# Performance work log

Measured on AMD Instinct MI355X. Metric: run time of the kernel, lower is better.

## Reference

```python
import jax, jax.numpy as jnp
import numpy as np

NUM_HEADS = 8


def setup_inputs() -> dict:
    key0 = jax.random.key(0)
    ks = jax.random.split(key0, 12)
    N, M, B, C = 512, 512, 1, 256
    inp = {
        "query": jax.random.normal(ks[0], (N, B, C), dtype=jnp.float32),
        "key": jax.random.normal(ks[1], (M, B, C), dtype=jnp.float32),
        "value": jax.random.normal(ks[2], (M, B, C), dtype=jnp.float32),
        "embed_g": jax.random.normal(ks[3], (B, N, M, C), dtype=jnp.float32),
        "Wq": jax.random.normal(ks[4], (C, C), dtype=jnp.float32) * 0.02,
        "bq": jnp.zeros((C,), dtype=jnp.float32),
        "Wk": jax.random.normal(ks[5], (C, C), dtype=jnp.float32) * 0.02,
        "bk": jnp.zeros((C,), dtype=jnp.float32),
        "Wv": jax.random.normal(ks[6], (C, C), dtype=jnp.float32) * 0.02,
        "bv": jnp.zeros((C,), dtype=jnp.float32),
        "Wg": jax.random.normal(ks[7], (C, C), dtype=jnp.float32) * 0.02,
        "bg": jnp.zeros((C,), dtype=jnp.float32),
    }
    return inp


def reference(query, key, value, embed_g, Wq, bq, Wk, bk, Wv, bv, Wg, bg):
    H = NUM_HEADS
    N, B, C = query.shape
    M = key.shape[0]
    Dh = C // H

    # torch nn.Linear: x @ W.T + b
    q = (query @ Wq.T + bq).reshape(N, B, H, Dh).transpose(1, 2, 0, 3)   # (B,H,N,Dh)
    k = (key @ Wk.T + bk).reshape(M, B, H, Dh).transpose(1, 2, 0, 3)     # (B,H,M,Dh)
    v = (value @ Wv.T + bv).reshape(M, B, H, Dh).transpose(1, 2, 0, 3)   # (B,H,M,Dh)
    g = (embed_g @ Wg.T + bg).reshape(B, N, M, H, Dh).transpose(0, 3, 1, 2, 4)  # (B,H,N,M,Dh)

    scores_p = jnp.einsum('bhnc,bhnmc->bhnm', q, g)
    scores_e = jnp.einsum('bhnc,bhmc->bhnm', q, k)
    scores = (scores_e + scores_p) / jnp.sqrt(jnp.asarray(Dh, dtype=q.dtype))
    attn = jax.nn.softmax(scores, axis=-1)                               # (B,H,N,M)

    hidden = jnp.einsum('bhnm,bhmd->bhnd', attn, v)                      # (B,H,N,Dh)
    hidden = hidden.transpose(0, 2, 1, 3).reshape(B, N, C)               # (B,N,C)
    hidden = hidden.transpose(1, 0, 2)                                   # (N,B,C)
    return hidden, attn
```

## Files before the change

### kernel.cpp

```cpp
#include <hip/hip_runtime.h>


template <int CTRL, int RMASK>
__device__ __forceinline__ float dpp_add(float v) {
  int x = __builtin_amdgcn_update_dpp(0, __float_as_int(v), CTRL, RMASK, 0xf, false);
  return v + __int_as_float(x);
}

__global__ __launch_bounds__(256) void k_transpose(const float* __restrict__ Wq,
                                                   const float* __restrict__ Wk,
                                                   const float* __restrict__ Wv,
                                                   float* __restrict__ wt) {
  const float* W = (blockIdx.y == 0) ? Wq : (blockIdx.y == 1) ? Wk : Wv;
  float* O = wt + (size_t)blockIdx.y * 65536;
  __shared__ float t[64][65];
  const int tile = blockIdx.x;
  const int tr = (tile >> 2) * 64, tc = (tile & 3) * 64;
  const int c = threadIdx.x & 63, r0 = threadIdx.x >> 6;
#pragma unroll
  for (int i = 0; i < 16; ++i) {
    int r = r0 + i * 4;
    t[r][c] = W[(tr + r) * 256 + tc + c];
  }
  __syncthreads();
#pragma unroll
  for (int i = 0; i < 16; ++i) {
    int r = r0 + i * 4;
    O[(tc + r) * 256 + tr + c] = t[c][r];
  }
}

__global__ __launch_bounds__(256) void k_proj(const float* __restrict__ q_in,
                                              const float* __restrict__ k_in,
                                              const float* __restrict__ v_in,
                                              const float* __restrict__ bq,
                                              const float* __restrict__ bk,
                                              const float* __restrict__ bv,
                                              const float* __restrict__ wt,
                                              float* __restrict__ outb) {
  const int mat = blockIdx.y;
  const float* x = mat == 0 ? q_in : mat == 1 ? k_in : v_in;
  const float* b = mat == 0 ? bq : mat == 1 ? bk : bv;
  const float* WT = wt + (size_t)mat * 65536;
  float* out = outb + (size_t)mat * 131072;

  __shared__ float xl[8][256];
  const int tid = threadIdx.x;
  const int n0 = blockIdx.x * 8;
  for (int idx = tid; idx < 2048; idx += 256)
    xl[idx >> 8][idx & 255] = x[(n0 + (idx >> 8)) * 256 + (idx & 255)];
  __syncthreads();

  float acc[8] = {0.f, 0.f, 0.f, 0.f, 0.f, 0.f, 0.f, 0.f};
  for (int j = 0; j < 256; j += 4) {
    const float w0 = WT[(j + 0) * 256 + tid];
    const float w1 = WT[(j + 1) * 256 + tid];
    const float w2 = WT[(j + 2) * 256 + tid];
    const float w3 = WT[(j + 3) * 256 + tid];
#pragma unroll
    for (int r = 0; r < 8; ++r) {
      const float4 xv = *(const float4*)&xl[r][j];
      acc[r] += xv.x * w0 + xv.y * w1 + xv.z * w2 + xv.w * w3;
    }
  }
  const float bb = b[tid];
#pragma unroll
  for (int r = 0; r < 8; ++r) out[(n0 + r) * 256 + tid] = acc[r] + bb;
}

__global__ __launch_bounds__(256) void k_tfold(const float* __restrict__ qkv,
                                               const float* __restrict__ Wg,
                                               const float* __restrict__ bg,
                                               float* __restrict__ t_ws,
                                               float* __restrict__ qb_ws) {
  const int h = blockIdx.y;
  const int n0 = blockIdx.x * 64;
  const int tid = threadIdx.x;
  __shared__ float wg_s[32][256];
  __shared__ float qs[64][32];
  __shared__ float bgs[32];

  for (int idx = tid; idx < 8192; idx += 256)
    wg_s[idx >> 8][idx & 255] = Wg[(size_t)(h * 32 + (idx >> 8)) * 256 + (idx & 255)];
  for (int idx = tid; idx < 2048; idx += 256)
    qs[idx >> 5][idx & 31] = qkv[(size_t)(n0 + (idx >> 5)) * 256 + h * 32 + (idx & 31)];
  if (tid < 32) bgs[tid] = bg[h * 32 + tid];
  __syncthreads();

  float wr[32];
#pragma unroll
  for (int i = 0; i < 32; ++i) wr[i] = wg_s[i][tid];
  for (int nn = 0; nn < 64; ++nn) {
    float a = 0.f;
#pragma unroll
    for (int i = 0; i < 32; ++i) a = fmaf(qs[nn][i], wr[i], a);
    t_ws[(size_t)(n0 + nn) * 2048 + h * 256 + tid] = a;
  }
  if (tid < 64) {
    float a = 0.f;
#pragma unroll
    for (int i = 0; i < 32; ++i) a = fmaf(qs[tid][i], bgs[i], a);
    qb_ws[(n0 + tid) * 8 + h] = a;
  }
}

__global__ __launch_bounds__(256) void k_scores(const float* __restrict__ Eg,
                                                const float* __restrict__ qkv,
                                                const float* __restrict__ t_ws,
                                                const float* __restrict__ qb_ws,
                                                float* __restrict__ attn_raw) {
  const int n = blockIdx.x, mb = blockIdx.y;
  const int tid = threadIdx.x;
  const int lane = tid & 63, w = tid >> 6;
  const int s = lane & 31, g = lane >> 5;
  const float* k_g = qkv + 131072;

  __shared__ float p_lds[1024];

  float t_r[8][8];
#pragma unroll
  for (int h = 0; h < 8; ++h) {
    const float4 a = *(const float4*)(t_ws + (size_t)n * 2048 + h * 256 + s * 8);
    const float4 b = *(const float4*)(t_ws + (size_t)n * 2048 + h * 256 + s * 8 + 4);
    t_r[h][0] = a.x; t_r[h][1] = a.y; t_r[h][2] = a.z; t_r[h][3] = a.w;
    t_r[h][4] = b.x; t_r[h][5] = b.y; t_r[h][6] = b.z; t_r[h][7] = b.w;
  }
  float q_r[8];
  {
    const float4 a = *(const float4*)(qkv + n * 256 + s * 8);
    const float4 b = *(const float4*)(qkv + n * 256 + s * 8 + 4);
    q_r[0] = a.x; q_r[1] = a.y; q_r[2] = a.z; q_r[3] = a.w;
    q_r[4] = b.x; q_r[5] = b.y; q_r[6] = b.z; q_r[7] = b.w;
  }
  float qb_r[8];
#pragma unroll
  for (int h = 0; h < 8; ++h) qb_r[h] = qb_ws[n * 8 + h];
  float msk[8];
#pragma unroll
  for (int h = 0; h < 8; ++h) msk[h] = ((s >> 2) == h) ? 1.f : 0.f;

  const float scale = 0.17677669529663687f;

  const int row0 = mb * 128 + w * 32 + g;
  const float* E0 = Eg + ((size_t)n * 512 + row0) * 256 + s * 8;
  const float* K0 = k_g + (size_t)row0 * 256 + s * 8;
  int mo = w * 32 + g;

#pragma unroll 2
  for (int it = 0; it < 16; ++it) {
    const float4 e0 = *(const float4*)(E0);
    const float4 e1 = *(const float4*)(E0 + 4);
    const float4 k0 = *(const float4*)(K0);
    const float4 k1 = *(const float4*)(K0 + 4);
    float kacc;
    kacc = k0.x * q_r[0];             kacc = fmaf(k0.y, q_r[1], kacc);
    kacc = fmaf(k0.z, q_r[2], kacc);  kacc = fmaf(k0.w, q_r[3], kacc);
    kacc = fmaf(k1.x, q_r[4], kacc);  kacc = fmaf(k1.y, q_r[5], kacc);
    kacc = fmaf(k1.z, q_r[6], kacc);  kacc = fmaf(k1.w, q_r[7], kacc);
#pragma unroll
    for (int h = 0; h < 8; ++h) {
      float v = msk[h] * kacc;
      v = fmaf(e0.x, t_r[h][0], v); v = fmaf(e0.y, t_r[h][1], v);
      v = fmaf(e0.z, t_r[h][2], v); v = fmaf(e0.w, t_r[h][3], v);
      v = fmaf(e1.x, t_r[h][4], v); v = fmaf(e1.y, t_r[h][5], v);
      v = fmaf(e1.z, t_r[h][6], v); v = fmaf(e1.w, t_r[h][7], v);
      v = dpp_add<0xB1, 0xf>(v);
      v = dpp_add<0x4E, 0xf>(v);
      v = dpp_add<0x141, 0xf>(v);
      v = dpp_add<0x140, 0xf>(v);
      v = dpp_add<0x142, 0xa>(v);
      v = (v + qb_r[h]) * scale;
      if (s == 16 + h) p_lds[h * 128 + mo] = v;
    }
    E0 += 512; K0 += 512; mo += 2;
  }
  __syncthreads();
  for (int idx = tid; idx < 1024; idx += 256)
    attn_raw[(size_t)(idx >> 7) * 262144 + n * 512 + mb * 128 + (idx & 127)] = p_lds[idx];
}

__global__ __launch_bounds__(512) void k_finish(const float* __restrict__ qkv,
                                                float* __restrict__ out) {
  const float* v_g = qkv + 262144;
  const int n = blockIdx.x, tid = threadIdx.x;
  const int lane = tid & 63, w = tid >> 6;
  float* attn = out + 131072;

  __shared__ float sc[4096];
  __shared__ float invd[8];
  __shared__ float pv[2][256];

  {
    float4* d = (float4*)sc;
    int i0 = tid;
    d[i0] = *(const float4*)(attn + (size_t)(i0 >> 7) * 262144 + n * 512 + (i0 & 127) * 4);
    int i1 = tid + 512;
    d[i1] = *(const float4*)(attn + (size_t)(i1 >> 7) * 262144 + n * 512 + (i1 & 127) * 4);
  }
  __syncthreads();

  {
    float vals[8];
#pragma unroll
    for (int i = 0; i < 8; ++i) vals[i] = sc[w * 512 + lane + i * 64];
    float mx = vals[0];
#pragma unroll
    for (int i = 1; i < 8; ++i) mx = fmaxf(mx, vals[i]);
#pragma unroll
    for (int off = 1; off < 64; off <<= 1) mx = fmaxf(mx, __shfl_xor(mx, off));
    float sum = 0.f;
#pragma unroll
    for (int i = 0; i < 8; ++i) {
      const float e = __expf(vals[i] - mx);
      sum += e;
      sc[w * 512 + lane + i * 64] = e;
    }
#pragma unroll
    for (int off = 1; off < 64; off <<= 1) sum += __shfl_xor(sum, off);
    if (lane == 0) invd[w] = 1.f / sum;
  }
  __syncthreads();

#pragma unroll
  for (int r = 0; r < 8; ++r) {
    const int idx = tid + r * 512;
    const int h = idx >> 9, m = idx & 511;
    attn[(size_t)h * 262144 + n * 512 + m] = sc[idx] * invd[h];
  }

  const int c = tid & 255, half = tid >> 8, h2 = c >> 5;
  const float* pr = sc + h2 * 512 + half * 256;
  const float* vp = v_g + (size_t)half * 65536 + c;
  float acc = 0.f;
#pragma unroll 4
  for (int m4 = 0; m4 < 64; ++m4) {
    const float4 p4 = *(const float4*)(pr + m4 * 4);
    const int mb = m4 * 4;
    acc = fmaf(p4.x, vp[(size_t)(mb + 0) * 256], acc);
    acc = fmaf(p4.y, vp[(size_t)(mb + 1) * 256], acc);
    acc = fmaf(p4.z, vp[(size_t)(mb + 2) * 256], acc);
    acc = fmaf(p4.w, vp[(size_t)(mb + 3) * 256], acc);
  }
  pv[half][c] = acc;
  __syncthreads();
  if (tid < 256) out[n * 256 + tid] = (pv[0][tid] + pv[1][tid]) * invd[tid >> 5];
}

extern "C" void kernel_launch(void* const* d_in, const int* in_sizes, int n_in,
                              void* d_out, int out_size, void* d_ws, size_t ws_size,
                              hipStream_t stream) {
  const float* query = (const float*)d_in[0];
  const float* key   = (const float*)d_in[1];
  const float* value = (const float*)d_in[2];
  const float* Eg    = (const float*)d_in[3];
  const float* Wq    = (const float*)d_in[4];
  const float* bq    = (const float*)d_in[5];
  const float* Wk    = (const float*)d_in[6];
  const float* bk    = (const float*)d_in[7];
  const float* Wv    = (const float*)d_in[8];
  const float* bv    = (const float*)d_in[9];
  const float* Wg    = (const float*)d_in[10];
  const float* bg    = (const float*)d_in[11];
  float* out = (float*)d_out;

  float* ws = (float*)d_ws;
  float* wt = ws;
  float* qkv = wt + 3 * 65536;
  float* t_ws = qkv + 3 * 131072;
  float* qb_ws = t_ws + 512 * 2048;

  k_transpose<<<dim3(16, 3), 256, 0, stream>>>(Wq, Wk, Wv, wt);
  k_proj<<<dim3(64, 3), 256, 0, stream>>>(query, key, value, bq, bk, bv, wt, qkv);
  k_tfold<<<dim3(8, 8), 256, 0, stream>>>(qkv, Wg, bg, t_ws, qb_ws);
  k_scores<<<dim3(512, 4), 256, 0, stream>>>(Eg, qkv, t_ws, qb_ws, out + 131072);
  k_finish<<<dim3(512), 512, 0, stream>>>(qkv, out);
}
```

Before: 113.1 us.

## Move q·k score term from scores kernel into finish kernel

Takes the q·k dot product out of the bandwidth-bound scores kernel and computes it once per (n,m) pair in the finish kernel, adding it into the shared-memory scores before the softmax. Previously every query row's block reloaded K and ran the per-head masked multiplies. The softmax scale is folded into t_ws and qb_ws in tfold and into q in finish, and the scores loop is unrolled more. The cost is an extra K read pass and one more barrier in the finish kernel.

```diff
diff --git a/kernel.cpp b/kernel.cpp
--- a/kernel.cpp
+++ b/kernel.cpp
@@ -76,6 +76,7 @@
   const int h = blockIdx.y;
   const int n0 = blockIdx.x * 64;
   const int tid = threadIdx.x;
+  const float scale = 0.17677669529663687f;
   __shared__ float wg_s[32][256];
   __shared__ float qs[64][32];
   __shared__ float bgs[32];
@@ -94,18 +95,17 @@
     float a = 0.f;
 #pragma unroll
     for (int i = 0; i < 32; ++i) a = fmaf(qs[nn][i], wr[i], a);
-    t_ws[(size_t)(n0 + nn) * 2048 + h * 256 + tid] = a;
+    t_ws[(size_t)(n0 + nn) * 2048 + h * 256 + tid] = a * scale;
   }
   if (tid < 64) {
     float a = 0.f;
 #pragma unroll
     for (int i = 0; i < 32; ++i) a = fmaf(qs[tid][i], bgs[i], a);
-    qb_ws[(n0 + tid) * 8 + h] = a;
+    qb_ws[(n0 + tid) * 8 + h] = a * scale;
   }
 }
 
 __global__ __launch_bounds__(256) void k_scores(const float* __restrict__ Eg,
-                                                const float* __restrict__ qkv,
                                                 const float* __restrict__ t_ws,
                                                 const float* __restrict__ qb_ws,
                                                 float* __restrict__ attn_raw) {
@@ -113,7 +113,6 @@
   const int tid = threadIdx.x;
   const int lane = tid & 63, w = tid >> 6;
   const int s = lane & 31, g = lane >> 5;
-  const float* k_g = qkv + 131072;
 
   __shared__ float p_lds[1024];
 
@@ -125,54 +124,34 @@
     t_r[h][0] = a.x; t_r[h][1] = a.y; t_r[h][2] = a.z; t_r[h][3] = a.w;
     t_r[h][4] = b.x; t_r[h][5] = b.y; t_r[h][6] = b.z; t_r[h][7] = b.w;
   }
-  float q_r[8];
-  {
-    const float4 a = *(const float4*)(qkv + n * 256 + s * 8);
-    const float4 b = *(const float4*)(qkv + n * 256 + s * 8 + 4);
-    q_r[0] = a.x; q_r[1] = a.y; q_r[2] = a.z; q_r[3] = a.w;
-    q_r[4] = b.x; q_r[5] = b.y; q_r[6] = b.z; q_r[7] = b.w;
-  }
   float qb_r[8];
 #pragma unroll
   for (int h = 0; h < 8; ++h) qb_r[h] = qb_ws[n * 8 + h];
-  float msk[8];
-#pragma unroll
-  for (int h = 0; h < 8; ++h) msk[h] = ((s >> 2) == h) ? 1.f : 0.f;
-
-  const float scale = 0.17677669529663687f;
 
   const int row0 = mb * 128 + w * 32 + g;
   const float* E0 = Eg + ((size_t)n * 512 + row0) * 256 + s * 8;
-  const float* K0 = k_g + (size_t)row0 * 256 + s * 8;
   int mo = w * 32 + g;
 
-#pragma unroll 2
+#pragma unroll 4
   for (int it = 0; it < 16; ++it) {
     const float4 e0 = *(const float4*)(E0);
     const float4 e1 = *(const float4*)(E0 + 4);
-    const float4 k0 = *(const float4*)(K0);
-    const float4 k1 = *(const float4*)(K0 + 4);
-    float kacc;
-    kacc = k0.x * q_r[0];             kacc = fmaf(k0.y, q_r[1], kacc);
-    kacc = fmaf(k0.z, q_r[2], kacc);  kacc = fmaf(k0.w, q_r[3], kacc);
-    kacc = fmaf(k1.x, q_r[4], kacc);  kacc = fmaf(k1.y, q_r[5], kacc);
-    kacc = fmaf(k1.z, q_r[6], kacc);  kacc = fmaf(k1.w, q_r[7], kacc);
 #pragma unroll
     for (int h = 0; h < 8; ++h) {
-      float v = msk[h] * kacc;
-      v = fmaf(e0.x, t_r[h][0], v); v = fmaf(e0.y, t_r[h][1], v);
-      v = fmaf(e0.z, t_r[h][2], v); v = fmaf(e0.w, t_r[h][3], v);
-      v = fmaf(e1.x, t_r[h][4], v); v = fmaf(e1.y, t_r[h][5], v);
-      v = fmaf(e1.z, t_r[h][6], v); v = fmaf(e1.w, t_r[h][7], v);
+      float v = e0.x * t_r[h][0];
+      v = fmaf(e0.y, t_r[h][1], v); v = fmaf(e0.z, t_r[h][2], v);
+      v = fmaf(e0.w, t_r[h][3], v); v = fmaf(e1.x, t_r[h][4], v);
+      v = fmaf(e1.y, t_r[h][5], v); v = fmaf(e1.z, t_r[h][6], v);
+      v = fmaf(e1.w, t_r[h][7], v);
       v = dpp_add<0xB1, 0xf>(v);
       v = dpp_add<0x4E, 0xf>(v);
       v = dpp_add<0x141, 0xf>(v);
       v = dpp_add<0x140, 0xf>(v);
       v = dpp_add<0x142, 0xa>(v);
-      v = (v + qb_r[h]) * scale;
+      v = v + qb_r[h];
       if (s == 16 + h) p_lds[h * 128 + mo] = v;
     }
-    E0 += 512; K0 += 512; mo += 2;
+    E0 += 512; mo += 2;
   }
   __syncthreads();
   for (int idx = tid; idx < 1024; idx += 256)
@@ -181,14 +160,25 @@
 
 __global__ __launch_bounds__(512) void k_finish(const float* __restrict__ qkv,
                                                 float* __restrict__ out) {
+  const float* k_g = qkv + 131072;
   const float* v_g = qkv + 262144;
   const int n = blockIdx.x, tid = threadIdx.x;
   const int lane = tid & 63, w = tid >> 6;
+  const int s = lane & 31, g = lane >> 5;
   float* attn = out + 131072;
 
   __shared__ float sc[4096];
   __shared__ float invd[8];
   __shared__ float pv[2][256];
+
+  float q_r[8];
+  {
+    const float scale = 0.17677669529663687f;
+    const float4 a = *(const float4*)(qkv + n * 256 + s * 8);
+    const float4 b = *(const float4*)(qkv + n * 256 + s * 8 + 4);
+    q_r[0] = a.x * scale; q_r[1] = a.y * scale; q_r[2] = a.z * scale; q_r[3] = a.w * scale;
+    q_r[4] = b.x * scale; q_r[5] = b.y * scale; q_r[6] = b.z * scale; q_r[7] = b.w * scale;
+  }
 
   {
     float4* d = (float4*)sc;
@@ -196,6 +186,25 @@
     d[i0] = *(const float4*)(attn + (size_t)(i0 >> 7) * 262144 + n * 512 + (i0 & 127) * 4);
     int i1 = tid + 512;
     d[i1] = *(const float4*)(attn + (size_t)(i1 >> 7) * 262144 + n * 512 + (i1 & 127) * 4);
+  }
+  __syncthreads();
+
+  {
+    const float* K0 = k_g + (size_t)(w * 64 + g) * 256 + s * 8;
+#pragma unroll 4
+    for (int it = 0; it < 32; ++it) {
+      const float4 k0 = *(const float4*)(K0);
+      const float4 k1 = *(const float4*)(K0 + 4);
+      float e = k0.x * q_r[0];
+      e = fmaf(k0.y, q_r[1], e); e = fmaf(k0.z, q_r[2], e);
+      e = fmaf(k0.w, q_r[3], e); e = fmaf(k1.x, q_r[4], e);
+      e = fmaf(k1.y, q_r[5], e); e = fmaf(k1.z, q_r[6], e);
+      e = fmaf(k1.w, q_r[7], e);
+      e = dpp_add<0xB1, 0xf>(e);
+      e = dpp_add<0x4E, 0xf>(e);
+      if ((s & 3) == 0) sc[(s >> 2) * 512 + (w * 64 + it * 2 + g)] += e;
+      K0 += 512;
+    }
   }
   __syncthreads();
 
@@ -272,6 +281,6 @@
   k_transpose<<<dim3(16, 3), 256, 0, stream>>>(Wq, Wk, Wv, wt);
   k_proj<<<dim3(64, 3), 256, 0, stream>>>(query, key, value, bq, bk, bv, wt, qkv);
   k_tfold<<<dim3(8, 8), 256, 0, stream>>>(qkv, Wg, bg, t_ws, qb_ws);
-  k_scores<<<dim3(512, 4), 256, 0, stream>>>(Eg, qkv, t_ws, qb_ws, out + 131072);
+  k_scores<<<dim3(512, 4), 256, 0, stream>>>(Eg, t_ws, qb_ws, out + 131072);
   k_finish<<<dim3(512), 512, 0, stream>>>(qkv, out);
 }
```

After: 121.4 us. 1.07x slower.

## Fuse score computation with softmax and PV into one per-row kernel

Applied to the files above, without the earlier changes.

Merges the scores kernel and the softmax/attention-times-V kernel into a single 512-thread block per query row. Raw scores stay in shared memory instead of making a round trip through global memory, and one kernel launch is removed. The scale factor is folded into the precomputed t, qb and q values. The trade-off is fewer, larger blocks (512 instead of 2048 score blocks), with each wave streaming twice as many rows of embed_g, which may reduce parallelism for the bandwidth-bound embed_g read.

```diff
diff --git a/kernel.cpp b/kernel.cpp
--- a/kernel.cpp
+++ b/kernel.cpp
@@ -76,6 +76,7 @@
   const int h = blockIdx.y;
   const int n0 = blockIdx.x * 64;
   const int tid = threadIdx.x;
+  const float scale = 0.17677669529663687f;
   __shared__ float wg_s[32][256];
   __shared__ float qs[64][32];
   __shared__ float bgs[32];
@@ -94,28 +95,33 @@
     float a = 0.f;
 #pragma unroll
     for (int i = 0; i < 32; ++i) a = fmaf(qs[nn][i], wr[i], a);
-    t_ws[(size_t)(n0 + nn) * 2048 + h * 256 + tid] = a;
+    t_ws[(size_t)(n0 + nn) * 2048 + h * 256 + tid] = a * scale;
   }
   if (tid < 64) {
     float a = 0.f;
 #pragma unroll
     for (int i = 0; i < 32; ++i) a = fmaf(qs[tid][i], bgs[i], a);
-    qb_ws[(n0 + tid) * 8 + h] = a;
-  }
-}
-
-__global__ __launch_bounds__(256) void k_scores(const float* __restrict__ Eg,
-                                                const float* __restrict__ qkv,
-                                                const float* __restrict__ t_ws,
-                                                const float* __restrict__ qb_ws,
-                                                float* __restrict__ attn_raw) {
-  const int n = blockIdx.x, mb = blockIdx.y;
+    qb_ws[(n0 + tid) * 8 + h] = a * scale;
+  }
+}
+
+__global__ __launch_bounds__(512, 4) void k_main(const float* __restrict__ Eg,
+                                                 const float* __restrict__ qkv,
+                                                 const float* __restrict__ t_ws,
+                                                 const float* __restrict__ qb_ws,
+                                                 float* __restrict__ out) {
+  const float* k_g = qkv + 131072;
+  const float* v_g = qkv + 262144;
+  const int n = blockIdx.x;
   const int tid = threadIdx.x;
   const int lane = tid & 63, w = tid >> 6;
   const int s = lane & 31, g = lane >> 5;
-  const float* k_g = qkv + 131072;
-
-  __shared__ float p_lds[1024];
+  const float scale = 0.17677669529663687f;
+  float* attn = out + 131072;
+
+  __shared__ float sc[4096];
+  __shared__ float invd[8];
+  __shared__ float pv[2][256];
 
   float t_r[8][8];
 #pragma unroll
@@ -129,8 +135,8 @@
   {
     const float4 a = *(const float4*)(qkv + n * 256 + s * 8);
     const float4 b = *(const float4*)(qkv + n * 256 + s * 8 + 4);
-    q_r[0] = a.x; q_r[1] = a.y; q_r[2] = a.z; q_r[3] = a.w;
-    q_r[4] = b.x; q_r[5] = b.y; q_r[6] = b.z; q_r[7] = b.w;
+    q_r[0] = a.x * scale; q_r[1] = a.y * scale; q_r[2] = a.z * scale; q_r[3] = a.w * scale;
+    q_r[4] = b.x * scale; q_r[5] = b.y * scale; q_r[6] = b.z * scale; q_r[7] = b.w * scale;
   }
   float qb_r[8];
 #pragma unroll
@@ -139,15 +145,12 @@
 #pragma unroll
   for (int h = 0; h < 8; ++h) msk[h] = ((s >> 2) == h) ? 1.f : 0.f;
 
-  const float scale = 0.17677669529663687f;
-
-  const int row0 = mb * 128 + w * 32 + g;
-  const float* E0 = Eg + ((size_t)n * 512 + row0) * 256 + s * 8;
-  const float* K0 = k_g + (size_t)row0 * 256 + s * 8;
-  int mo = w * 32 + g;
+  const float* E0 = Eg + ((size_t)n * 512 + w * 64 + g) * 256 + s * 8;
+  const float* K0 = k_g + (size_t)(w * 64 + g) * 256 + s * 8;
+  int m = w * 64 + g;
 
 #pragma unroll 2
-  for (int it = 0; it < 16; ++it) {
+  for (int it = 0; it < 32; ++it) {
     const float4 e0 = *(const float4*)(E0);
     const float4 e1 = *(const float4*)(E0 + 4);
     const float4 k0 = *(const float4*)(K0);
@@ -169,33 +172,9 @@
       v = dpp_add<0x141, 0xf>(v);
       v = dpp_add<0x140, 0xf>(v);
       v = dpp_add<0x142, 0xa>(v);
-      v = (v + qb_r[h]) * scale;
-      if (s == 16 + h) p_lds[h * 128 + mo] = v;
+      if (s == 16 + h) sc[h * 512 + m] = v + qb_r[h];
     }
-    E0 += 512; K0 += 512; mo += 2;
-  }
-  __syncthreads();
-  for (int idx = tid; idx < 1024; idx += 256)
-    attn_raw[(size_t)(idx >> 7) * 262144 + n * 512 + mb * 128 + (idx & 127)] = p_lds[idx];
-}
-
-__global__ __launch_bounds__(512) void k_finish(const float* __restrict__ qkv,
-                                                float* __restrict__ out) {
-  const float* v_g = qkv + 262144;
-  const int n = blockIdx.x, tid = threadIdx.x;
-  const int lane = tid & 63, w = tid >> 6;
-  float* attn = out + 131072;
-
-  __shared__ float sc[4096];
-  __shared__ float invd[8];
-  __shared__ float pv[2][256];
-
-  {
-    float4* d = (float4*)sc;
-    int i0 = tid;
-    d[i0] = *(const float4*)(attn + (size_t)(i0 >> 7) * 262144 + n * 512 + (i0 & 127) * 4);
-    int i1 = tid + 512;
-    d[i1] = *(const float4*)(attn + (size_t)(i1 >> 7) * 262144 + n * 512 + (i1 & 127) * 4);
+    E0 += 512; K0 += 512; m += 2;
   }
   __syncthreads();
 
@@ -224,8 +203,8 @@
 #pragma unroll
   for (int r = 0; r < 8; ++r) {
     const int idx = tid + r * 512;
-    const int h = idx >> 9, m = idx & 511;
-    attn[(size_t)h * 262144 + n * 512 + m] = sc[idx] * invd[h];
+    const int h = idx >> 9, mm = idx & 511;
+    attn[(size_t)h * 262144 + n * 512 + mm] = sc[idx] * invd[h];
   }
 
   const int c = tid & 255, half = tid >> 8, h2 = c >> 5;
@@ -272,6 +251,5 @@
   k_transpose<<<dim3(16, 3), 256, 0, stream>>>(Wq, Wk, Wv, wt);
   k_proj<<<dim3(64, 3), 256, 0, stream>>>(query, key, value, bq, bk, bv, wt, qkv);
   k_tfold<<<dim3(8, 8), 256, 0, stream>>>(qkv, Wg, bg, t_ws, qb_ws);
-  k_scores<<<dim3(512, 4), 256, 0, stream>>>(Eg, qkv, t_ws, qb_ws, out + 131072);
-  k_finish<<<dim3(512), 512, 0, stream>>>(qkv, out);
-}
+  k_main<<<dim3(512), 512, 0, stream>>>(Eg, qkv, t_ws, qb_ws, out);
+}
```

Result: faster. 105.8 us (-6.5%).
